# Kernel tuning notes

Hardware: AMD Instinct MI355X
Metric: run time of the kernel (lower is better)

The kernel has to match this reference:

```python
import jax, jax.numpy as jnp
import numpy as np

MAX_ROUNDS = 6
MIN_ROUNDS = 2
WINDOW = 4
LAMBDA_P = 0.2
LN_EPS = 1e-5


def _mlp(x, W1, b1, W2, b2):
    # Linear -> exact GELU -> Linear (matches nn.Sequential(Linear, GELU, Linear))
    return jax.nn.gelu(x @ W1 + b1, approximate=False) @ W2 + b2


def _layernorm(x, g, b):
    m = x.mean(-1, keepdims=True)
    v = x.var(-1, keepdims=True)
    return (x - m) / jnp.sqrt(v + LN_EPS) * g + b


def setup_inputs() -> dict:
    key = jax.random.key(0)
    ks = jax.random.split(key, 13)
    B, N, D = 4, 2048, 512
    s = 0.02
    f32 = jnp.float32
    return {
        "summaries": jax.random.normal(ks[0], (B, N, D), f32),
        "msg_W1": jax.random.normal(ks[1], (2 * D, D), f32) * s,
        "msg_b1": jnp.zeros((D,), f32),
        "msg_W2": jax.random.normal(ks[2], (D, D), f32) * s,
        "msg_b2": jnp.zeros((D,), f32),
        "upd_W1": jax.random.normal(ks[3], (2 * D, D), f32) * s,
        "upd_b1": jnp.zeros((D,), f32),
        "upd_W2": jax.random.normal(ks[4], (D, D), f32) * s,
        "upd_b2": jnp.zeros((D,), f32),
        "halt_W": jax.random.normal(ks[5], (D, 1), f32) * s,
        "halt_b": jnp.zeros((1,), f32),
        "ln_g": jnp.ones((D,), f32),
        "ln_b": jnp.zeros((D,), f32),
    }


def reference(summaries, msg_W1, msg_b1, msg_W2, msg_b2,
              upd_W1, upd_b1, upd_W2, upd_b2,
              halt_W, halt_b, ln_g, ln_b):
    B, N, D = summaries.shape
    dt = summaries.dtype
    h = summaries
    remaining = jnp.ones((B, N, 1), dt)
    output = jnp.zeros_like(h)
    kl = jnp.zeros((), dt)
    done = jnp.asarray(False)  # emulates the early `break` under jit
    pos = jnp.arange(N)
    # number of valid causal neighbors of position i: min(i+1, window+1)
    counts = jnp.minimum(pos + 1, WINDOW + 1).astype(dt)[None, :, None]

    for step in range(MAX_ROUNDS):
        # windowed gather + message MLP, vectorized over the (W+1) offsets
        acc = jnp.zeros_like(h)
        for d in range(WINDOW + 1):
            nb = h if d == 0 else jnp.pad(h, ((0, 0), (d, 0), (0, 0)))[:, :N]
            m = _mlp(jnp.concatenate([h, nb], axis=-1), msg_W1, msg_b1, msg_W2, msg_b2)
            mask = (pos >= d).astype(dt)[None, :, None]
            acc = acc + m * mask
        msgs = acc / counts  # mean over valid neighbors, shape (B, N, D)

        new_h = h + _mlp(jnp.concatenate([h, msgs], axis=-1), upd_W1, upd_b1, upd_W2, upd_b2)
        h_next = _layernorm(new_h, ln_g, ln_b)

        if step < MIN_ROUNDS:
            halt = jnp.zeros((B, N, 1), dt)
        elif step == MAX_ROUNDS - 1:
            halt = jnp.ones((B, N, 1), dt)
        else:
            hp = jax.nn.sigmoid(h_next.mean(axis=1, keepdims=True) @ halt_W + halt_b)  # (B,1,1)
            halt = jnp.broadcast_to(hp, (B, N, 1))

        step_weight = remaining * halt
        out_next = output + step_weight * h_next
        rem_next = remaining * (1.0 - halt)

        p_geom = LAMBDA_P * (1.0 - LAMBDA_P) ** step
        # F.kl_div(log(q), log(p), log_target=True) = p * (log p - log q)
        kl_term = p_geom * (jnp.log(p_geom) - jnp.log(halt.mean() + 1e-8))

        active = jnp.logical_not(done)
        af = active.astype(dt)
        h = jnp.where(active, h_next, h)
        output = jnp.where(active, out_next, output)
        remaining = jnp.where(active, rem_next, remaining)
        kl = kl + af * kl_term.astype(dt)
        done = jnp.logical_or(done, remaining.max() < 0.01)

    return output, kl / MAX_ROUNDS
```

## Files before the change

### kernel.cpp

```cpp
#include <hip/hip_runtime.h>
#include <cmath>

#define DEV __device__ __forceinline__

typedef __bf16 bf16x8 __attribute__((ext_vector_type(8)));
typedef float f32x4v __attribute__((ext_vector_type(4)));
typedef unsigned short u16x8 __attribute__((ext_vector_type(8)));
typedef unsigned short u16x4 __attribute__((ext_vector_type(4)));

DEV float bf2f(unsigned short u){ return __uint_as_float(((unsigned)u)<<16); }
DEV unsigned short f2bf(float f){
  unsigned u = __float_as_uint(f);
  u = (u + 0x7fffu + ((u>>16)&1u)) >> 16;
  return (unsigned short)u;
}
DEV float geluf(float x){ return 0.5f*x*(1.0f + erff(x*0.7071067811865475f)); }

#define GLDS16(g,l) __builtin_amdgcn_global_load_lds(\
    (const __attribute__((address_space(1))) void*)(g), \
    (__attribute__((address_space(3))) void*)(l), 16, 0, 0)

#define NB    4
#define NSEQ  2048
#define DDIM  512
#define MROWS 8192

#define OFF_H     0u
#define OFF_HB    16777216u
#define OFF_UV    25165824u
#define OFF_GP    25165824u
#define OFF_R     33554432u
#define OFF_GSC   41943040u
#define OFF_WUV   50331648u
#define OFF_WP    51380224u
#define OFF_WR    52428800u
#define OFF_BUV   52953088u
#define OFF_BP    52957184u
#define OFF_BR    52959232u
#define OFF_DOT   52961280u
#define OFF_SCAL  52994048u
#define OFF_FLAGS 52994112u

__global__ __launch_bounds__(256) void k_prep_wt(
    const float* __restrict__ mW1, const float* __restrict__ uW2,
    const float* __restrict__ uW1, const float* __restrict__ mb1,
    const float* __restrict__ ub2,
    unsigned short* __restrict__ Wuv, unsigned short* __restrict__ Wr,
    unsigned short* __restrict__ Wp, float* __restrict__ biasUV,
    float* __restrict__ biasR)
{
  int idx = blockIdx.x*256 + threadIdx.x;
  if (idx < 524288){
    int n = idx>>9, k = idx&511;
    float v = (n<512) ? mW1[k*512+n] : mW1[(512+k)*512 + (n-512)];
    Wuv[idx] = f2bf(v);
  } else if (idx < 786432){
    int j = idx-524288; int n=j>>9, k=j&511;
    Wr[j] = f2bf(uW2[k*512+n]);
  } else if (idx < 1048576){
    int j = idx-786432; int n=j>>9, k=j&511;
    Wp[n*1024+k] = f2bf(uW1[k*512+n]);
  } else if (idx < 1049600){
    int j = idx-1048576; biasUV[j] = (j<512)? mb1[j] : 0.f;
  } else {
    int j = idx-1049600; biasR[j] = ub2[j];
  }
}

__global__ __launch_bounds__(256) void k_prep_m2u(
    const float* __restrict__ mW2, const float* __restrict__ uW1,
    unsigned short* __restrict__ Wp)
{
  int a = blockIdx.x>>1;
  int n = ((blockIdx.x&1)<<8) + threadIdx.x;
  float s = 0.f;
  for (int j=0;j<512;++j) s += mW2[a*512+j]*uW1[(512+j)*512+n];
  Wp[n*1024 + 512 + a] = f2bf(s);
}

__global__ __launch_bounds__(256) void k_prep_biasP(
    const float* __restrict__ ub1, const float* __restrict__ mb2,
    const float* __restrict__ uW1, float* __restrict__ biasP)
{
  int n = blockIdx.x*256 + threadIdx.x;
  float s = ub1[n];
  for (int j=0;j<512;++j) s += mb2[j]*uW1[(512+j)*512+n];
  biasP[n] = s;
}

__global__ void k_init_state(float* scal, int* flags){
  int t = threadIdx.x;
  if (t<4) scal[t]=1.f;
  else if (t<9) scal[t]=0.f;
  if (t==9){ flags[0]=1; flags[1]=0; }
}

__global__ __launch_bounds__(256) void k_init_h(
    const float* __restrict__ S, float* __restrict__ H, u16x4* __restrict__ Hb)
{
  size_t idx = (size_t)blockIdx.x*256 + threadIdx.x;
  float4 v = ((const float4*)S)[idx];
  ((float4*)H)[idx] = v;
  u16x4 o; o[0]=f2bf(v.x); o[1]=f2bf(v.y); o[2]=f2bf(v.z); o[3]=f2bf(v.w);
  Hb[idx] = o;
}

template<int EPI>
__global__ __launch_bounds__(256) void k_gemm(
    const unsigned short* __restrict__ A0, const unsigned short* __restrict__ A1,
    const unsigned short* __restrict__ Bt, const float* __restrict__ bias,
    void* __restrict__ Cout, int N, int ldb, int nK, int ksplit, int gridN,
    const int* __restrict__ flags)
{
  if (flags[0]==0) return;
  __shared__ unsigned short sm[2][12288];
  const int tid = threadIdx.x;
  const int bid = blockIdx.x;
  const int xcd = bid & 7, ib = bid >> 3;
  const int ppx = (int)(gridDim.x >> 3) / gridN;
  const int m0 = (xcd*ppx + ib/gridN) << 7;
  const int n0 = (ib % gridN) << 6;
  const int sr = tid>>3;
  const int scA = (((tid&7) ^ (sr&7)) << 3);
  const int lane = tid&63, wv = tid>>6, wr = wv>>1, wc = wv&1;
  const int la = lane&15, lg = lane>>4;
  const int swzr = (la&7)<<3;
  f32x4v acc[4][2] = {};

  auto stage = [&](int ks, int bufi){
    const unsigned short* As = (ks<ksplit)? A0 : A1;
    const int kc = ((ks<ksplit)? ks : (ks-ksplit))<<6;
    unsigned short* s = sm[bufi];
    #pragma unroll
    for (int i=0;i<4;++i)
      GLDS16(As + (size_t)(m0 + i*32 + sr)*512 + kc + scA, s + i*2048 + tid*8);
    #pragma unroll
    for (int i=0;i<2;++i)
      GLDS16(Bt + (size_t)(n0 + i*32 + sr)*ldb + (ks<<6) + scA, s + 8192 + i*2048 + tid*8);
  };

  stage(0, 0);
  __syncthreads();
  int buf = 0;
  for (int ks=0; ks<nK; ++ks){
    if (ks+1 < nK) stage(ks+1, buf^1);
    const unsigned short* s = sm[buf];
    #pragma unroll
    for (int kk=0;kk<2;++kk){
      bf16x8 af[4], bfr[2];
      #pragma unroll
      for (int mi=0;mi<4;++mi)
        af[mi] = *(const bf16x8*)(s + ((wr<<6) + (mi<<4) + la)*64 + (((kk<<5) + (lg<<3)) ^ swzr));
      #pragma unroll
      for (int ni=0;ni<2;++ni)
        bfr[ni] = *(const bf16x8*)(s + 8192 + ((wc<<5) + (ni<<4) + la)*64 + (((kk<<5) + (lg<<3)) ^ swzr));
      #pragma unroll
      for (int mi=0;mi<4;++mi)
        #pragma unroll
        for (int ni=0;ni<2;++ni)
          acc[mi][ni] = __builtin_amdgcn_mfma_f32_16x16x32_bf16(af[mi], bfr[ni], acc[mi][ni], 0, 0, 0);
    }
    __syncthreads();
    buf ^= 1;
  }

  const int r0 = m0 + (wr<<6) + (lg<<2);
  const int c0 = n0 + (wc<<5) + la;
  #pragma unroll
  for (int mi=0;mi<4;++mi){
    #pragma unroll
    for (int ni=0;ni<2;++ni){
      const int col = c0 + (ni<<4);
      const float bs = bias[col];
      #pragma unroll
      for (int r=0;r<4;++r){
        const int row = r0 + (mi<<4) + r;
        float v = acc[mi][ni][r] + bs;
        if constexpr (EPI==1) v = geluf(v);
        if constexpr (EPI==2) ((float*)Cout)[(size_t)row*N + col] = v;
        else ((unsigned short*)Cout)[(size_t)row*N + col] = f2bf(v);
      }
    }
  }
}

__global__ __launch_bounds__(256) void k_geluacc(
    const unsigned short* __restrict__ UV, unsigned short* __restrict__ G,
    const int* __restrict__ flags)
{
  if (flags[0]==0) return;
  int r = blockIdx.x*4 + (threadIdx.x>>6);
  int lane = threadIdx.x & 63;
  int c8 = lane*8;
  int i = r & (NSEQ-1);
  int nd = (i<4) ? i : 4;
  const u16x8 u = *(const u16x8*)(UV + (size_t)r*1024 + c8);
  float acc[8] = {0,0,0,0,0,0,0,0};
  for (int d=0; d<=nd; ++d){
    const u16x8 v = *(const u16x8*)(UV + (size_t)(r-d)*1024 + 512 + c8);
    #pragma unroll
    for (int j=0;j<8;++j) acc[j] += geluf(bf2f(u[j]) + bf2f(v[j]));
  }
  float inv = 1.0f/(float)(nd+1);
  u16x8 o;
  #pragma unroll
  for (int j=0;j<8;++j) o[j] = f2bf(acc[j]*inv);
  *(u16x8*)(G + (size_t)r*512 + c8) = o;
}

__global__ __launch_bounds__(256) void k_ln(
    const float* __restrict__ Rr, float* __restrict__ H, unsigned short* __restrict__ Hb,
    const float* __restrict__ gamma, const float* __restrict__ beta,
    const float* __restrict__ hW, float* __restrict__ DOT, float* __restrict__ OUT,
    const float* __restrict__ scal, const int* __restrict__ flags,
    int accmode, int dodot)
{
  const int lane = threadIdx.x & 63;
  const int row = (blockIdx.x<<2) + (threadIdx.x>>6);
  const int bidx = row >> 11;
  const size_t base = (size_t)row*512 + lane*8;
  float4 x0 = *(const float4*)(H+base);
  float4 x1 = *(const float4*)(H+base+4);

  if (accmode){
    const float w = scal[4+bidx];
    float4 o0, o1;
    if (accmode==1){
      o0 = make_float4(w*x0.x, w*x0.y, w*x0.z, w*x0.w);
      o1 = make_float4(w*x1.x, w*x1.y, w*x1.z, w*x1.w);
    } else {
      o0 = *(const float4*)(OUT+base);
      o1 = *(const float4*)(OUT+base+4);
      o0.x += w*x0.x; o0.y += w*x0.y; o0.z += w*x0.z; o0.w += w*x0.w;
      o1.x += w*x1.x; o1.y += w*x1.y; o1.z += w*x1.z; o1.w += w*x1.w;
    }
    *(float4*)(OUT+base)   = o0;
    *(float4*)(OUT+base+4) = o1;
  }
  if (flags[0]==0) return;

  float4 r0 = *(const float4*)(Rr+base);
  float4 r1 = *(const float4*)(Rr+base+4);
  x0.x+=r0.x; x0.y+=r0.y; x0.z+=r0.z; x0.w+=r0.w;
  x1.x+=r1.x; x1.y+=r1.y; x1.z+=r1.z; x1.w+=r1.w;
  float s = x0.x+x0.y+x0.z+x0.w + x1.x+x1.y+x1.z+x1.w;
  float q = x0.x*x0.x+x0.y*x0.y+x0.z*x0.z+x0.w*x0.w
          + x1.x*x1.x+x1.y*x1.y+x1.z*x1.z+x1.w*x1.w;
  #pragma unroll
  for (int off=1; off<64; off<<=1){ s += __shfl_xor(s, off); q += __shfl_xor(q, off); }
  const float mean = s*(1.f/512.f);
  const float var  = q*(1.f/512.f) - mean*mean;
  const float rstd = rsqrtf(var + 1e-5f);
  float4 g0 = *(const float4*)(gamma + lane*8);
  float4 g1 = *(const float4*)(gamma + lane*8 + 4);
  float4 b0 = *(const float4*)(beta  + lane*8);
  float4 b1 = *(const float4*)(beta  + lane*8 + 4);
  float y[8];
  y[0]=(x0.x-mean)*rstd*g0.x+b0.x; y[1]=(x0.y-mean)*rstd*g0.y+b0.y;
  y[2]=(x0.z-mean)*rstd*g0.z+b0.z; y[3]=(x0.w-mean)*rstd*g0.w+b0.w;
  y[4]=(x1.x-mean)*rstd*g1.x+b1.x; y[5]=(x1.y-mean)*rstd*g1.y+b1.y;
  y[6]=(x1.z-mean)*rstd*g1.z+b1.z; y[7]=(x1.w-mean)*rstd*g1.w+b1.w;
  *(float4*)(H+base)   = make_float4(y[0],y[1],y[2],y[3]);
  *(float4*)(H+base+4) = make_float4(y[4],y[5],y[6],y[7]);
  u16x8 hb;
  #pragma unroll
  for (int j=0;j<8;++j) hb[j] = f2bf(y[j]);
  *(u16x8*)(Hb+base) = hb;

  if (dodot){
    float4 w0 = *(const float4*)(hW + lane*8);
    float4 w1 = *(const float4*)(hW + lane*8 + 4);
    float d = y[0]*w0.x + y[1]*w0.y + y[2]*w0.z + y[3]*w0.w
            + y[4]*w1.x + y[5]*w1.y + y[6]*w1.z + y[7]*w1.w;
    #pragma unroll
    for (int off=1; off<64; off<<=1) d += __shfl_xor(d, off);
    if (lane==0) DOT[row] = d;
  }
}

__global__ void k_control(const float* __restrict__ DOT, const float* __restrict__ hb,
                          float* __restrict__ scal, int* __restrict__ flags,
                          int step, float p, float logp, float* __restrict__ klout)
{
  __shared__ float hp[4];
  const int t = threadIdx.x, lane = t&63, b = t>>6;
  if (step>=2 && step<5){
    float s = 0.f;
    for (int i=lane; i<NSEQ; i+=64) s += DOT[b*NSEQ + i];
    #pragma unroll
    for (int off=1; off<64; off<<=1) s += __shfl_xor(s, off);
    if (lane==0) hp[b] = s;
  } else if (lane==0) hp[b] = 0.f;
  __syncthreads();
  if (t==0){
    bool active = flags[0]!=0;
    float halt[NB];
    for (int i=0;i<NB;++i){
      if (step < 2) halt[i]=0.f;
      else if (step == 5) halt[i]=1.f;
      else { float z = hp[i]*(1.f/2048.f) + hb[0]; halt[i] = 1.f/(1.f+expf(-z)); }
    }
    float hm = 0.25f*(halt[0]+halt[1]+halt[2]+halt[3]);
    if (active) scal[8] += p*(logp - logf(hm + 1e-8f));
    float mx = 0.f;
    for (int i=0;i<NB;++i){
      float rb = scal[i];
      float w  = active ? rb*halt[i] : 0.f;
      scal[4+i] = w;
      if (active) rb *= (1.f - halt[i]);
      scal[i] = rb;
      mx = fmaxf(mx, rb);
    }
    if (mx < 0.01f) flags[1] = 1;
    flags[0] = flags[1] ? 0 : 1;
    if (step==5) *klout = scal[8]*(1.0f/6.0f);
  }
}

__global__ __launch_bounds__(256) void k_accum(
    const float* __restrict__ H, const float* __restrict__ scal, float* __restrict__ OUT)
{
  size_t idx = (size_t)blockIdx.x*256 + threadIdx.x;
  int b = (int)(idx >> 18);
  float w = scal[4+b];
  float4 h = ((const float4*)H)[idx];
  float4 o = ((float4*)OUT)[idx];
  ((float4*)OUT)[idx] = make_float4(o.x+w*h.x, o.y+w*h.y, o.z+w*h.z, o.w+w*h.w);
}

extern "C" void kernel_launch(void* const* d_in, const int* in_sizes, int n_in,
                              void* d_out, int out_size, void* d_ws, size_t ws_size,
                              hipStream_t stream)
{
  const float* S   = (const float*)d_in[0];
  const float* mW1 = (const float*)d_in[1];
  const float* mb1 = (const float*)d_in[2];
  const float* mW2 = (const float*)d_in[3];
  const float* mb2 = (const float*)d_in[4];
  const float* uW1 = (const float*)d_in[5];
  const float* ub1 = (const float*)d_in[6];
  const float* uW2 = (const float*)d_in[7];
  const float* ub2 = (const float*)d_in[8];
  const float* hW  = (const float*)d_in[9];
  const float* hb  = (const float*)d_in[10];
  const float* lng = (const float*)d_in[11];
  const float* lnb = (const float*)d_in[12];

  char* ws = (char*)d_ws;
  float*          H     = (float*)(ws + OFF_H);
  unsigned short* Hb    = (unsigned short*)(ws + OFF_HB);
  unsigned short* UV    = (unsigned short*)(ws + OFF_UV);
  unsigned short* GP    = (unsigned short*)(ws + OFF_GP);
  unsigned short* GSC   = (unsigned short*)(ws + OFF_GSC);
  float*          Rb    = (float*)(ws + OFF_R);
  unsigned short* Wuv   = (unsigned short*)(ws + OFF_WUV);
  unsigned short* Wp    = (unsigned short*)(ws + OFF_WP);
  unsigned short* Wr    = (unsigned short*)(ws + OFF_WR);
  float*          biasUV= (float*)(ws + OFF_BUV);
  float*          biasP = (float*)(ws + OFF_BP);
  float*          biasR = (float*)(ws + OFF_BR);
  float*          DOT   = (float*)(ws + OFF_DOT);
  float*          scal  = (float*)(ws + OFF_SCAL);
  int*            flags = (int*)(ws + OFF_FLAGS);
  float*          OUT   = (float*)d_out;
  float*          klout = OUT + (size_t)NB*NSEQ*DDIM;

  k_prep_wt   <<<4102, 256, 0, stream>>>(mW1, uW2, uW1, mb1, ub2, Wuv, Wr, Wp, biasUV, biasR);
  k_prep_m2u  <<<1024, 256, 0, stream>>>(mW2, uW1, Wp);
  k_prep_biasP<<<2,    256, 0, stream>>>(ub1, mb2, uW1, biasP);
  k_init_state<<<1,    256, 0, stream>>>(scal, flags);
  k_init_h    <<<4096, 256, 0, stream>>>(S, H, (u16x4*)Hb);

  for (int s = 0; s < 6; ++s){
    k_gemm<0><<<1024, 256, 0, stream>>>(Hb, Hb, Wuv, biasUV, UV, 1024, 512, 8, 8, 16, flags);
    k_geluacc<<<2048, 256, 0, stream>>>(UV, GSC, flags);
    k_gemm<1><<<512, 256, 0, stream>>>(Hb, GSC, Wp, biasP, GP, 512, 1024, 16, 8, 8, flags);
    k_gemm<2><<<512, 256, 0, stream>>>(GP, GP, Wr, biasR, Rb, 512, 512, 8, 8, 8, flags);
    const int accmode = (s==3) ? 1 : (s>=4 ? 2 : 0);
    const int dodot   = (s>=2 && s<=4) ? 1 : 0;
    k_ln<<<2048, 256, 0, stream>>>(Rb, H, Hb, lng, lnb, hW, DOT, OUT, scal, flags, accmode, dodot);
    float p = 0.2f * (float)pow(0.8, (double)s);
    float lp = (float)log((double)p);
    k_control<<<1, 256, 0, stream>>>(DOT, hb, scal, flags, s, p, lp, klout);
  }
  k_accum<<<4096, 256, 0, stream>>>(H, scal, OUT);
}
```

Measured before the change: 592.9 us.

## Widen GEMM tiles to 128x128, drop double buffering, and speed up weight prep

The GEMM tile grows from 128x64 to 128x128 with a single shared-memory buffer instead of double buffering, so each block reuses more A data and fewer blocks are launched. The weight prep now uses an LDS-tiled transpose kernel, and the fused msg_W2·upd_W1 product is computed with the MFMA GEMM instead of a scalar loop. The wider tiles give fewer blocks per GEMM, which may leave CUs underused on 256-CU hardware. Removing double buffering exposes global-load latency in the K loop.

Measured after the change: 655.3 us. 1.11x slower.

```diff
diff --git a/kernel.cpp b/kernel.cpp
--- a/kernel.cpp
+++ b/kernel.cpp
@@ -40,42 +40,43 @@
 #define OFF_DOT   52961280u
 #define OFF_SCAL  52994048u
 #define OFF_FLAGS 52994112u
-
-__global__ __launch_bounds__(256) void k_prep_wt(
+#define OFF_A2    25165824u
+#define OFF_B2    25690112u
+
+__global__ __launch_bounds__(256) void k_prep_tr(
     const float* __restrict__ mW1, const float* __restrict__ uW2,
-    const float* __restrict__ uW1, const float* __restrict__ mb1,
+    const float* __restrict__ uW1,
+    unsigned short* __restrict__ Wuv, unsigned short* __restrict__ Wr,
+    unsigned short* __restrict__ Wp,  unsigned short* __restrict__ A2)
+{
+  __shared__ float t[64][65];
+  const int tid = threadIdx.x, c = tid&63, r4 = tid>>6;
+  const float* src; unsigned short* dst; int dld;
+  switch (blockIdx.y){
+    case 0: src = mW1;          dst = Wuv;          dld = 512;  break;
+    case 1: src = mW1 + 262144; dst = Wuv + 262144; dld = 512;  break;
+    case 2: src = uW2;          dst = Wr;           dld = 512;  break;
+    case 3: src = uW1;          dst = Wp;           dld = 1024; break;
+    default:src = uW1 + 262144; dst = A2;           dld = 512;  break;
+  }
+  const int k0 = (blockIdx.x>>3)<<6, n0 = (blockIdx.x&7)<<6;
+  #pragma unroll
+  for (int i=0;i<16;++i){ int r = i*4 + r4; t[r][c] = src[(size_t)(k0+r)*512 + n0 + c]; }
+  __syncthreads();
+  #pragma unroll
+  for (int i=0;i<16;++i){ int r = i*4 + r4; dst[(size_t)(n0+r)*dld + k0 + c] = f2bf(t[c][r]); }
+}
+
+__global__ __launch_bounds__(256) void k_prep_small(
+    const float* __restrict__ mW2, const float* __restrict__ mb1,
     const float* __restrict__ ub2,
-    unsigned short* __restrict__ Wuv, unsigned short* __restrict__ Wr,
-    unsigned short* __restrict__ Wp, float* __restrict__ biasUV,
+    unsigned short* __restrict__ B2, float* __restrict__ biasUV,
     float* __restrict__ biasR)
 {
   int idx = blockIdx.x*256 + threadIdx.x;
-  if (idx < 524288){
-    int n = idx>>9, k = idx&511;
-    float v = (n<512) ? mW1[k*512+n] : mW1[(512+k)*512 + (n-512)];
-    Wuv[idx] = f2bf(v);
-  } else if (idx < 786432){
-    int j = idx-524288; int n=j>>9, k=j&511;
-    Wr[j] = f2bf(uW2[k*512+n]);
-  } else if (idx < 1048576){
-    int j = idx-786432; int n=j>>9, k=j&511;
-    Wp[n*1024+k] = f2bf(uW1[k*512+n]);
-  } else if (idx < 1049600){
-    int j = idx-1048576; biasUV[j] = (j<512)? mb1[j] : 0.f;
-  } else {
-    int j = idx-1049600; biasR[j] = ub2[j];
-  }
-}
-
-__global__ __launch_bounds__(256) void k_prep_m2u(
-    const float* __restrict__ mW2, const float* __restrict__ uW1,
-    unsigned short* __restrict__ Wp)
-{
-  int a = blockIdx.x>>1;
-  int n = ((blockIdx.x&1)<<8) + threadIdx.x;
-  float s = 0.f;
-  for (int j=0;j<512;++j) s += mW2[a*512+j]*uW1[(512+j)*512+n];
-  Wp[n*1024 + 512 + a] = f2bf(s);
+  if (idx < 262144)      B2[idx] = f2bf(mW2[idx]);
+  else if (idx < 263168){ int j = idx-262144; biasUV[j] = (j<512)? mb1[j] : 0.f; }
+  else if (idx < 263680){ int j = idx-263168; biasR[j] = ub2[j]; }
 }
 
 __global__ __launch_bounds__(256) void k_prep_biasP(
@@ -109,67 +110,60 @@
 __global__ __launch_bounds__(256) void k_gemm(
     const unsigned short* __restrict__ A0, const unsigned short* __restrict__ A1,
     const unsigned short* __restrict__ Bt, const float* __restrict__ bias,
-    void* __restrict__ Cout, int N, int ldb, int nK, int ksplit, int gridN,
+    void* __restrict__ Cout, int ldc, int ldb, int nK, int ksplit, int gridN,
     const int* __restrict__ flags)
 {
   if (flags[0]==0) return;
-  __shared__ unsigned short sm[2][12288];
+  __shared__ unsigned short sm[16384];
   const int tid = threadIdx.x;
   const int bid = blockIdx.x;
-  const int xcd = bid & 7, ib = bid >> 3;
-  const int ppx = (int)(gridDim.x >> 3) / gridN;
-  const int m0 = (xcd*ppx + ib/gridN) << 7;
-  const int n0 = (ib % gridN) << 6;
+  const int nb  = (int)gridDim.x;
+  const int ppx = (nb>>3)/gridN;
+  int mp, np;
+  if (ppx*gridN*8 == nb){ const int xcd = bid&7, ib = bid>>3; mp = xcd*ppx + ib/gridN; np = ib%gridN; }
+  else                  { mp = bid/gridN; np = bid%gridN; }
+  const int m0 = mp<<7, n0 = np<<7;
   const int sr = tid>>3;
   const int scA = (((tid&7) ^ (sr&7)) << 3);
   const int lane = tid&63, wv = tid>>6, wr = wv>>1, wc = wv&1;
   const int la = lane&15, lg = lane>>4;
   const int swzr = (la&7)<<3;
-  f32x4v acc[4][2] = {};
-
-  auto stage = [&](int ks, int bufi){
+  f32x4v acc[4][4] = {};
+
+  for (int ks=0; ks<nK; ++ks){
     const unsigned short* As = (ks<ksplit)? A0 : A1;
     const int kc = ((ks<ksplit)? ks : (ks-ksplit))<<6;
-    unsigned short* s = sm[bufi];
     #pragma unroll
     for (int i=0;i<4;++i)
-      GLDS16(As + (size_t)(m0 + i*32 + sr)*512 + kc + scA, s + i*2048 + tid*8);
-    #pragma unroll
-    for (int i=0;i<2;++i)
-      GLDS16(Bt + (size_t)(n0 + i*32 + sr)*ldb + (ks<<6) + scA, s + 8192 + i*2048 + tid*8);
-  };
-
-  stage(0, 0);
-  __syncthreads();
-  int buf = 0;
-  for (int ks=0; ks<nK; ++ks){
-    if (ks+1 < nK) stage(ks+1, buf^1);
-    const unsigned short* s = sm[buf];
+      GLDS16(As + (size_t)(m0 + i*32 + sr)*512 + kc + scA, sm + i*2048 + tid*8);
+    #pragma unroll
+    for (int i=0;i<4;++i)
+      GLDS16(Bt + (size_t)(n0 + i*32 + sr)*ldb + (ks<<6) + scA, sm + 8192 + i*2048 + tid*8);
+    __syncthreads();
     #pragma unroll
     for (int kk=0;kk<2;++kk){
-      bf16x8 af[4], bfr[2];
+      bf16x8 af[4], bfr[4];
       #pragma unroll
       for (int mi=0;mi<4;++mi)
-        af[mi] = *(const bf16x8*)(s + ((wr<<6) + (mi<<4) + la)*64 + (((kk<<5) + (lg<<3)) ^ swzr));
+        af[mi] = *(const bf16x8*)(sm + ((wr<<6) + (mi<<4) + la)*64 + (((kk<<5) + (lg<<3)) ^ swzr));
       #pragma unroll
-      for (int ni=0;ni<2;++ni)
-        bfr[ni] = *(const bf16x8*)(s + 8192 + ((wc<<5) + (ni<<4) + la)*64 + (((kk<<5) + (lg<<3)) ^ swzr));
+      for (int ni=0;ni<4;++ni)
+        bfr[ni] = *(const bf16x8*)(sm + 8192 + ((wc<<6) + (ni<<4) + la)*64 + (((kk<<5) + (lg<<3)) ^ swzr));
       #pragma unroll
       for (int mi=0;mi<4;++mi)
         #pragma unroll
-        for (int ni=0;ni<2;++ni)
+        for (int ni=0;ni<4;++ni)
           acc[mi][ni] = __builtin_amdgcn_mfma_f32_16x16x32_bf16(af[mi], bfr[ni], acc[mi][ni], 0, 0, 0);
     }
     __syncthreads();
-    buf ^= 1;
   }
 
   const int r0 = m0 + (wr<<6) + (lg<<2);
-  const int c0 = n0 + (wc<<5) + la;
+  const int c0 = n0 + (wc<<6) + la;
   #pragma unroll
   for (int mi=0;mi<4;++mi){
     #pragma unroll
-    for (int ni=0;ni<2;++ni){
+    for (int ni=0;ni<4;++ni){
       const int col = c0 + (ni<<4);
       const float bs = bias[col];
       #pragma unroll
@@ -177,8 +171,8 @@
         const int row = r0 + (mi<<4) + r;
         float v = acc[mi][ni][r] + bs;
         if constexpr (EPI==1) v = geluf(v);
-        if constexpr (EPI==2) ((float*)Cout)[(size_t)row*N + col] = v;
-        else ((unsigned short*)Cout)[(size_t)row*N + col] = f2bf(v);
+        if constexpr (EPI==2) ((float*)Cout)[(size_t)row*ldc + col] = v;
+        else ((unsigned short*)Cout)[(size_t)row*ldc + col] = f2bf(v);
       }
     }
   }
@@ -356,6 +350,8 @@
   unsigned short* Wuv   = (unsigned short*)(ws + OFF_WUV);
   unsigned short* Wp    = (unsigned short*)(ws + OFF_WP);
   unsigned short* Wr    = (unsigned short*)(ws + OFF_WR);
+  unsigned short* A2    = (unsigned short*)(ws + OFF_A2);
+  unsigned short* B2    = (unsigned short*)(ws + OFF_B2);
   float*          biasUV= (float*)(ws + OFF_BUV);
   float*          biasP = (float*)(ws + OFF_BP);
   float*          biasR = (float*)(ws + OFF_BR);
@@ -365,17 +361,18 @@
   float*          OUT   = (float*)d_out;
   float*          klout = OUT + (size_t)NB*NSEQ*DDIM;
 
-  k_prep_wt   <<<4102, 256, 0, stream>>>(mW1, uW2, uW1, mb1, ub2, Wuv, Wr, Wp, biasUV, biasR);
-  k_prep_m2u  <<<1024, 256, 0, stream>>>(mW2, uW1, Wp);
+  k_init_state<<<1, 256, 0, stream>>>(scal, flags);
+  k_prep_tr   <<<dim3(64,5), 256, 0, stream>>>(mW1, uW2, uW1, Wuv, Wr, Wp, A2);
+  k_prep_small<<<1032, 256, 0, stream>>>(mW2, mb1, ub2, B2, biasUV, biasR);
   k_prep_biasP<<<2,    256, 0, stream>>>(ub1, mb2, uW1, biasP);
-  k_init_state<<<1,    256, 0, stream>>>(scal, flags);
+  k_gemm<0><<<16, 256, 0, stream>>>(A2, A2, B2, biasUV+512, Wp+512, 1024, 512, 8, 8, 4, flags);
   k_init_h    <<<4096, 256, 0, stream>>>(S, H, (u16x4*)Hb);
 
   for (int s = 0; s < 6; ++s){
-    k_gemm<0><<<1024, 256, 0, stream>>>(Hb, Hb, Wuv, biasUV, UV, 1024, 512, 8, 8, 16, flags);
+    k_gemm<0><<<512, 256, 0, stream>>>(Hb, Hb, Wuv, biasUV, UV, 1024, 512, 8, 8, 8, flags);
     k_geluacc<<<2048, 256, 0, stream>>>(UV, GSC, flags);
-    k_gemm<1><<<512, 256, 0, stream>>>(Hb, GSC, Wp, biasP, GP, 512, 1024, 16, 8, 8, flags);
-    k_gemm<2><<<512, 256, 0, stream>>>(GP, GP, Wr, biasR, Rb, 512, 512, 8, 8, 8, flags);
+    k_gemm<1><<<256, 256, 0, stream>>>(Hb, GSC, Wp, biasP, GP, 512, 1024, 16, 8, 4, flags);
+    k_gemm<2><<<256, 256, 0, stream>>>(GP, GP, Wr, biasR, Rb, 512, 512, 8, 8, 4, flags);
     const int accmode = (s==3) ? 1 : (s>=4 ? 2 : 0);
     const int dodot   = (s>=2 && s<=4) ? 1 : 0;
     k_ln<<<2048, 256, 0, stream>>>(Rb, H, Hb, lng, lnb, hW, DOT, OUT, scal, flags, accmode, dodot);
```
